# Kernel optimization log

Hardware: AMD Instinct MI355X
Metric: run time of the kernel (lower is better)

The kernel has to match this reference:

```python
import jax, jax.numpy as jnp
import numpy as np

B, C, T_TEXT, T_FEAT = 32, 256, 512, 2048
DELTA = 0.1  # self.temperature


def setup_inputs() -> dict:
    key = jax.random.key(0)
    k1, k2 = jax.random.split(key)
    x = jax.random.normal(k1, (B, C, T_TEXT), dtype=jnp.float32)
    # token durations in frames, ~U[0, 8): avg ~4 frames/token -> T_FEAT ~ 2048
    w = jax.random.uniform(k2, (B, T_TEXT), dtype=jnp.float32) * 8.0
    x_mask = jnp.ones((B, T_TEXT), dtype=bool)
    y_mask = jnp.ones((B, T_FEAT), dtype=bool)
    return {"x": x, "w": w, "x_mask": x_mask, "y_mask": y_mask}


def reference(x, w, x_mask, y_mask):
    # Gaussian upsampling (arXiv 2010.04301) with fixed temperature DELTA.
    # x: (B, C, T_text), w: (B, T_text), x_mask: (B, T_text), y_mask: (B, T_feat)
    T_feats = y_mask.shape[-1]
    # frame time indices, zeroed where y_mask is False
    t = jnp.arange(T_feats, dtype=jnp.float32)[None, :] * y_mask.astype(jnp.float32)  # (B, T_feat)
    # Gaussian centers: cumulative duration minus half of own duration
    c = jnp.cumsum(w, axis=-1) - 0.5 * w  # (B, T_text)
    # energy: -delta * (t - c)^2  -> (B, T_feat, T_text)
    energy = -DELTA * (t[:, :, None] - c[:, None, :]) ** 2
    # mask out padded text tokens
    energy = jnp.where(x_mask[:, None, :], energy, -jnp.inf)
    p_attn = jax.nn.softmax(energy, axis=-1)  # (B, T_feat, T_text)
    # weighted sum over text tokens: (B, C, T_feat)
    out = jnp.einsum("btn,bcn->bct", p_attn, x)
    return out
```

## Files before the change

kernel.cpp:

```cpp
#include <hip/hip_runtime.h>
#include <hip/hip_bf16.h>

#define B_    32
#define C_    256
#define NT    512
#define TFEAT 2048
#define TT    32
#define UW    96
#define PRE   32
#define DELTA 0.1f
#define PSTR  104
#define TPB   2
#define NGRP  32
#define TSTR  36

typedef __attribute__((ext_vector_type(4))) float f32x4;
typedef __attribute__((ext_vector_type(8))) unsigned short u16x8;
typedef __attribute__((ext_vector_type(8))) __bf16 bf16x8;

static __device__ inline unsigned short f2bfbits(float f) {
    __bf16 h = (__bf16)f;
    return __builtin_bit_cast(unsigned short, h);
}
static __device__ inline float bf2f(unsigned short h) {
    return __uint_as_float(((unsigned)h) << 16);
}

__global__ __launch_bounds__(256, 2) void fused_kernel(const float* __restrict__ x,
                                                       const float* __restrict__ w,
                                                       float* __restrict__ out) {
    __shared__ float cs[NT];
    __shared__ float wsum[8];
    __shared__ unsigned short Pt[TT][PSTR];
    __shared__ float Sinv[TT];
    __shared__ int sLO[TPB];
    __shared__ float trans[4][16][TSTR];

    int tid  = threadIdx.x;
    int bx   = blockIdx.x;
    int b    = bx & 31;
    int grp  = bx >> 5;
    int lane = tid & 63;
    int wv   = tid >> 6;

    float v0 = w[b * NT + tid];
    float v1 = w[b * NT + 256 + tid];
    float s0 = v0, s1 = v1;
#pragma unroll
    for (int off = 1; off < 64; off <<= 1) {
        float t0 = __shfl_up(s0, off);
        float t1 = __shfl_up(s1, off);
        if (lane >= off) { s0 += t0; s1 += t1; }
    }
    if (lane == 63) { wsum[wv] = s0; wsum[4 + wv] = s1; }
    __syncthreads();
    float pre0 = 0.f;
    float pre1 = wsum[0] + wsum[1] + wsum[2] + wsum[3];
#pragma unroll
    for (int i = 0; i < 4; ++i) if (i < wv) pre0 += wsum[i];
#pragma unroll
    for (int i = 0; i < 4; ++i) if (i < wv) pre1 += wsum[4 + i];
    cs[tid]       = pre0 + s0 - 0.5f * v0;
    cs[256 + tid] = pre1 + s1 - 0.5f * v1;
    __syncthreads();

    if (wv == 0) {
        int gid = lane >> 4;
        int k   = lane & 15;
        if (gid < TPB) {
            float ft = (float)((grp * TPB + gid) * TT);
            bool p = cs[32 * k + 31] < ft;
            unsigned long long m = __ballot(p);
            int K = __popcll((m >> (gid * 16)) & 0xFFFFull);
            int n;
            if (K >= 16) {
                n = NT;
            } else {
                int base = 32 * K;
                bool pa = cs[base + k] < ft;
                bool pb = cs[base + 16 + k] < ft;
                unsigned long long ma = __ballot(pa);
                unsigned long long mb = __ballot(pb);
                n = base + __popcll((ma >> (gid * 16)) & 0xFFFFull)
                         + __popcll((mb >> (gid * 16)) & 0xFFFFull);
            }
            if (k == 0) {
                int n1 = n < NT - 1 ? n : NT - 1;
                int n0 = n - 1 > 0 ? n - 1 : 0;
                int nstar = (fabsf(ft - cs[n0]) <= fabsf(ft - cs[n1])) ? n0 : n1;
                int L = (nstar - PRE) & ~3;
                if (L < 0) L = 0;
                if (L > NT - UW) L = NT - UW;
                sLO[gid] = L;
            }
        }
    }
    __syncthreads();

    int g = tid >> 3, j = tid & 7;
    int arow = lane & 15, kg = lane >> 4;
    int rr = lane >> 3, tq = lane & 7;

    for (int it = 0; it < TPB; ++it) {
        {
            int LO = sLO[it];
            float ft = (float)((grp * TPB + it) * TT + g);
            float e[12];
            float mx = -1e30f;
#pragma unroll
            for (int k = 0; k < 12; ++k) {
                float d = ft - cs[LO + j + 8 * k];
                e[k] = -DELTA * d * d;
                mx = fmaxf(mx, e[k]);
            }
            mx = fmaxf(mx, __shfl_xor(mx, 1));
            mx = fmaxf(mx, __shfl_xor(mx, 2));
            mx = fmaxf(mx, __shfl_xor(mx, 4));
            float sum = 0.f;
#pragma unroll
            for (int k = 0; k < 12; ++k) {
                unsigned short pbv = f2bfbits(__expf(e[k] - mx));
                sum += bf2f(pbv);
                Pt[g][j + 8 * k] = pbv;
            }
            sum += __shfl_xor(sum, 1);
            sum += __shfl_xor(sum, 2);
            sum += __shfl_xor(sum, 4);
            if (j == 0) Sinv[g] = 1.f / fmaxf(sum, 1e-30f);
        }
        __syncthreads();

        int LO = sLO[it];

        bf16x8 pfrag[2][3];
#pragma unroll
        for (int tt = 0; tt < 2; ++tt)
#pragma unroll
            for (int ks = 0; ks < 3; ++ks)
                pfrag[tt][ks] = __builtin_bit_cast(bf16x8,
                    *reinterpret_cast<const u16x8*>(
                        &Pt[tt * 16 + arow][ks * 32 + kg * 8]));

        f32x4 acc[2][4];
#pragma unroll
        for (int tt = 0; tt < 2; ++tt)
#pragma unroll
            for (int m = 0; m < 4; ++m)
                acc[tt][m] = (f32x4){0.f, 0.f, 0.f, 0.f};

        const float* xb = x + ((size_t)b * C_) * NT + LO + kg * 8;
#pragma unroll
        for (int m = 0; m < 4; ++m) {
            const float* xr = xb + (size_t)(wv * 64 + m * 16 + arow) * NT;
            bf16x8 xf[3];
#pragma unroll
            for (int ks = 0; ks < 3; ++ks) {
                f32x4 a0 = *reinterpret_cast<const f32x4*>(xr + ks * 32);
                f32x4 a1 = *reinterpret_cast<const f32x4*>(xr + ks * 32 + 4);
                bf16x8 vv;
#pragma unroll
                for (int q = 0; q < 4; ++q) {
                    vv[q]     = (__bf16)a0[q];
                    vv[q + 4] = (__bf16)a1[q];
                }
                xf[ks] = vv;
            }
#pragma unroll
            for (int tt = 0; tt < 2; ++tt)
#pragma unroll
                for (int ks = 0; ks < 3; ++ks)
                    acc[tt][m] = __builtin_amdgcn_mfma_f32_16x16x32_bf16(
                        pfrag[tt][ks], xf[ks], acc[tt][m], 0, 0, 0);
        }

        int t0f = (grp * TPB + it) * TT;
        float* ob = out + ((size_t)b * C_) * TFEAT + t0f;
        f32x4 sv0 = *reinterpret_cast<const f32x4*>(&Sinv[kg * 4]);
        f32x4 sv1 = *reinterpret_cast<const f32x4*>(&Sinv[16 + kg * 4]);
#pragma unroll
        for (int m = 0; m < 4; ++m) {
            *reinterpret_cast<f32x4*>(&trans[wv][arow][kg * 4])      = acc[0][m] * sv0;
            *reinterpret_cast<f32x4*>(&trans[wv][arow][16 + kg * 4]) = acc[1][m] * sv1;
            f32x4 o0 = *reinterpret_cast<const f32x4*>(&trans[wv][rr][tq * 4]);
            f32x4 o1 = *reinterpret_cast<const f32x4*>(&trans[wv][8 + rr][tq * 4]);
            int c0 = wv * 64 + m * 16;
            *reinterpret_cast<f32x4*>(ob + (size_t)(c0 + rr) * TFEAT + tq * 4)     = o0;
            *reinterpret_cast<f32x4*>(ob + (size_t)(c0 + 8 + rr) * TFEAT + tq * 4) = o1;
        }
        __syncthreads();
    }
}

extern "C" void kernel_launch(void* const* d_in, const int* in_sizes, int n_in,
                              void* d_out, int out_size, void* d_ws, size_t ws_size,
                              hipStream_t stream) {
    const float* x = (const float*)d_in[0];
    const float* w = (const float*)d_in[1];
    float* out = (float*)d_out;

    hipLaunchKernelGGL(fused_kernel, dim3(B_ * NGRP), dim3(256), 0, stream,
                       x, w, out);
}
```

Before: 34.86 us.

## Split into attention-weight kernel and GEMM kernel with x cached in LDS

Splits the fused kernel into two launches. The first computes the normalized banded bf16 attention weights and window offsets per 32-frame tile and writes them to workspace. The second keeps a 16-channel slab of x for a batch in shared memory as bf16 and loops over all 64 tiles. It reads the precomputed weights and writes output through an LDS staging buffer with nontemporal stores. This removes the old kernel's repeated per-tile global reads and bf16 conversion of x, at the cost of an extra launch and a workspace round trip for the weights. If the workspace is too small, it falls back to the old fused kernel.

```diff
diff --git a/kernel.cpp b/kernel.cpp
--- a/kernel.cpp
+++ b/kernel.cpp
@@ -10,25 +10,229 @@
 #define PRE   32
 #define DELTA 0.1f
 #define PSTR  104
+#define XSTR  520
+#define OSTR  516
+
+#define PHAT_ELEMS ((size_t)B_ * 64 * TT * UW)
+#define WS_NEED (PHAT_ELEMS * 2 + (size_t)B_ * 64 * 4)
+
+typedef __attribute__((ext_vector_type(4))) float f32x4;
+typedef __attribute__((ext_vector_type(8))) unsigned short u16x8;
+typedef __attribute__((ext_vector_type(8))) __bf16 bf16x8;
+
+static __device__ inline unsigned short f2bfbits(float f) {
+    __bf16 h = (__bf16)f;
+    return __builtin_bit_cast(unsigned short, h);
+}
+static __device__ inline float bf2f(unsigned short h) {
+    return __uint_as_float(((unsigned)h) << 16);
+}
+
+__global__ __launch_bounds__(256, 2) void p_kernel(const float* __restrict__ w,
+                                                   unsigned short* __restrict__ phat,
+                                                   int* __restrict__ lotab) {
+    __shared__ float cs[NT];
+    __shared__ float wsum[8];
+    __shared__ unsigned short Pt[TT][PSTR];
+    __shared__ int sLO[4];
+
+    int tid  = threadIdx.x;
+    int bx   = blockIdx.x;
+    int b    = bx & 31;
+    int tg   = bx >> 5;
+    int lane = tid & 63;
+    int wv   = tid >> 6;
+
+    float v0 = w[b * NT + tid];
+    float v1 = w[b * NT + 256 + tid];
+    float s0 = v0, s1 = v1;
+#pragma unroll
+    for (int off = 1; off < 64; off <<= 1) {
+        float t0 = __shfl_up(s0, off);
+        float t1 = __shfl_up(s1, off);
+        if (lane >= off) { s0 += t0; s1 += t1; }
+    }
+    if (lane == 63) { wsum[wv] = s0; wsum[4 + wv] = s1; }
+    __syncthreads();
+    float pre0 = 0.f;
+    float pre1 = wsum[0] + wsum[1] + wsum[2] + wsum[3];
+#pragma unroll
+    for (int i = 0; i < 4; ++i) if (i < wv) pre0 += wsum[i];
+#pragma unroll
+    for (int i = 0; i < 4; ++i) if (i < wv) pre1 += wsum[4 + i];
+    cs[tid]       = pre0 + s0 - 0.5f * v0;
+    cs[256 + tid] = pre1 + s1 - 0.5f * v1;
+    __syncthreads();
+
+    if (wv == 0) {
+        int gid = lane >> 4;
+        int k   = lane & 15;
+        float ft = (float)((tg * 4 + gid) * TT);
+        bool p = cs[32 * k + 31] < ft;
+        unsigned long long m = __ballot(p);
+        int K = __popcll((m >> (gid * 16)) & 0xFFFFull);
+        int n;
+        if (K >= 16) {
+            n = NT;
+        } else {
+            int base = 32 * K;
+            bool pa = cs[base + k] < ft;
+            bool pb = cs[base + 16 + k] < ft;
+            unsigned long long ma = __ballot(pa);
+            unsigned long long mb = __ballot(pb);
+            n = base + __popcll((ma >> (gid * 16)) & 0xFFFFull)
+                     + __popcll((mb >> (gid * 16)) & 0xFFFFull);
+        }
+        if (k == 0) {
+            int n1 = n < NT - 1 ? n : NT - 1;
+            int n0 = n - 1 > 0 ? n - 1 : 0;
+            int nstar = (fabsf(ft - cs[n0]) <= fabsf(ft - cs[n1])) ? n0 : n1;
+            int L = (nstar - PRE) & ~3;
+            if (L < 0) L = 0;
+            if (L > NT - UW) L = NT - UW;
+            sLO[gid] = L;
+            lotab[b * 64 + tg * 4 + gid] = L;
+        }
+    }
+    __syncthreads();
+
+    int g = tid >> 3, j = tid & 7;
+
+    for (int it = 0; it < 4; ++it) {
+        int tile = tg * 4 + it;
+        int LO = sLO[it];
+        float ft = (float)(tile * TT + g);
+        float e[12];
+        float mx = -1e30f;
+#pragma unroll
+        for (int k = 0; k < 12; ++k) {
+            float d = ft - cs[LO + j + 8 * k];
+            e[k] = -DELTA * d * d;
+            mx = fmaxf(mx, e[k]);
+        }
+        mx = fmaxf(mx, __shfl_xor(mx, 1));
+        mx = fmaxf(mx, __shfl_xor(mx, 2));
+        mx = fmaxf(mx, __shfl_xor(mx, 4));
+        float p[12];
+        float sum = 0.f;
+#pragma unroll
+        for (int k = 0; k < 12; ++k) {
+            p[k] = __expf(e[k] - mx);
+            sum += p[k];
+        }
+        sum += __shfl_xor(sum, 1);
+        sum += __shfl_xor(sum, 2);
+        sum += __shfl_xor(sum, 4);
+        float inv = 1.f / fmaxf(sum, 1e-30f);
+#pragma unroll
+        for (int k = 0; k < 12; ++k)
+            Pt[g][j + 8 * k] = f2bfbits(p[k] * inv);
+        __syncthreads();
+
+        const unsigned* pw = (const unsigned*)&Pt[0][0];
+        unsigned* gd = (unsigned*)phat + (size_t)(b * 64 + tile) * 1536 + tid * 6;
+        int a = tid >> 3, r6 = tid & 7;
+#pragma unroll
+        for (int q = 0; q < 6; ++q)
+            gd[q] = pw[a * (PSTR / 2) + r6 * 6 + q];
+        __syncthreads();
+    }
+}
+
+__global__ __launch_bounds__(256, 2) void g_kernel(const float* __restrict__ x,
+                                                   const unsigned short* __restrict__ phat,
+                                                   const int* __restrict__ lotab,
+                                                   float* __restrict__ out) {
+    __shared__ unsigned short xs[16][XSTR];
+    __shared__ float outbuf[16][OSTR];
+
+    int tid  = threadIdx.x;
+    int bx   = blockIdx.x;
+    int b    = bx & 31;
+    int cg   = bx >> 5;
+    int c0   = cg * 16;
+    int lane = tid & 63;
+    int w    = tid >> 6;
+
+    {
+        int c = tid >> 4, k = tid & 15;
+        const float* xr = x + ((size_t)(b * C_ + c0 + c)) * NT + k * 32;
+#pragma unroll
+        for (int jj = 0; jj < 4; ++jj) {
+            f32x4 a0 = *reinterpret_cast<const f32x4*>(xr + jj * 8);
+            f32x4 a1 = *reinterpret_cast<const f32x4*>(xr + jj * 8 + 4);
+            bf16x8 vv;
+#pragma unroll
+            for (int q = 0; q < 4; ++q) {
+                vv[q]     = (__bf16)a0[q];
+                vv[q + 4] = (__bf16)a1[q];
+            }
+            *reinterpret_cast<bf16x8*>(&xs[c][k * 32 + jj * 8]) = vv;
+        }
+    }
+    __syncthreads();
+
+    int cc = lane & 15;
+    int kg = lane >> 4;
+
+    for (int s = 0; s < 16; ++s) {
+        int tile = s * 4 + w;
+        int LO = lotab[b * 64 + tile];
+
+        const unsigned short* ap = phat + (size_t)(b * 64 + tile) * (TT * UW);
+        bf16x8 af[2][3];
+#pragma unroll
+        for (int mt = 0; mt < 2; ++mt)
+#pragma unroll
+            for (int ks = 0; ks < 3; ++ks)
+                af[mt][ks] = __builtin_bit_cast(bf16x8,
+                    *reinterpret_cast<const u16x8*>(
+                        ap + (mt * 16 + cc) * UW + ks * 32 + kg * 8));
+
+        bf16x8 bfg[3];
+#pragma unroll
+        for (int ks = 0; ks < 3; ++ks)
+            bfg[ks] = __builtin_bit_cast(bf16x8,
+                *reinterpret_cast<const u16x8*>(&xs[cc][LO + ks * 32 + kg * 8]));
+
+        f32x4 acc[2];
+        acc[0] = (f32x4){0.f, 0.f, 0.f, 0.f};
+        acc[1] = (f32x4){0.f, 0.f, 0.f, 0.f};
+#pragma unroll
+        for (int mt = 0; mt < 2; ++mt)
+#pragma unroll
+            for (int ks = 0; ks < 3; ++ks)
+                acc[mt] = __builtin_amdgcn_mfma_f32_16x16x32_bf16(
+                    af[mt][ks], bfg[ks], acc[mt], 0, 0, 0);
+
+        int toff = (s & 3) * 128 + w * 32 + kg * 4;
+#pragma unroll
+        for (int mt = 0; mt < 2; ++mt)
+            *reinterpret_cast<f32x4*>(&outbuf[cc][toff + mt * 16]) = acc[mt];
+
+        if ((s & 3) == 3) {
+            __syncthreads();
+            int row = tid >> 4, kk = tid & 15;
+            int tb = (s >> 2) * 512;
+            float* ob = out + ((size_t)(b * C_ + c0 + row)) * TFEAT + tb;
+#pragma unroll
+            for (int jj = 0; jj < 8; ++jj) {
+                f32x4 v = *reinterpret_cast<const f32x4*>(&outbuf[row][(kk + 16 * jj) * 4]);
+                __builtin_nontemporal_store(v,
+                    reinterpret_cast<f32x4*>(ob + (kk + 16 * jj) * 4));
+            }
+            __syncthreads();
+        }
+    }
+}
+
 #define TPB   2
 #define NGRP  32
 #define TSTR  36
 
-typedef __attribute__((ext_vector_type(4))) float f32x4;
-typedef __attribute__((ext_vector_type(8))) unsigned short u16x8;
-typedef __attribute__((ext_vector_type(8))) __bf16 bf16x8;
-
-static __device__ inline unsigned short f2bfbits(float f) {
-    __bf16 h = (__bf16)f;
-    return __builtin_bit_cast(unsigned short, h);
-}
-static __device__ inline float bf2f(unsigned short h) {
-    return __uint_as_float(((unsigned)h) << 16);
-}
-
-__global__ __launch_bounds__(256, 2) void fused_kernel(const float* __restrict__ x,
-                                                       const float* __restrict__ w,
-                                                       float* __restrict__ out) {
+__global__ __launch_bounds__(256, 2) void fused_fallback(const float* __restrict__ x,
+                                                         const float* __restrict__ w,
+                                                         float* __restrict__ out) {
     __shared__ float cs[NT];
     __shared__ float wsum[8];
     __shared__ unsigned short Pt[TT][PSTR];
@@ -131,7 +335,6 @@
         __syncthreads();
 
         int LO = sLO[it];
-
         bf16x8 pfrag[2][3];
 #pragma unroll
         for (int tt = 0; tt < 2; ++tt)
@@ -183,9 +386,9 @@
             *reinterpret_cast<f32x4*>(&trans[wv][arow][16 + kg * 4]) = acc[1][m] * sv1;
             f32x4 o0 = *reinterpret_cast<const f32x4*>(&trans[wv][rr][tq * 4]);
             f32x4 o1 = *reinterpret_cast<const f32x4*>(&trans[wv][8 + rr][tq * 4]);
-            int c0 = wv * 64 + m * 16;
-            *reinterpret_cast<f32x4*>(ob + (size_t)(c0 + rr) * TFEAT + tq * 4)     = o0;
-            *reinterpret_cast<f32x4*>(ob + (size_t)(c0 + 8 + rr) * TFEAT + tq * 4) = o1;
+            int cq = wv * 64 + m * 16;
+            *reinterpret_cast<f32x4*>(ob + (size_t)(cq + rr) * TFEAT + tq * 4)     = o0;
+            *reinterpret_cast<f32x4*>(ob + (size_t)(cq + 8 + rr) * TFEAT + tq * 4) = o1;
         }
         __syncthreads();
     }
@@ -198,6 +401,14 @@
     const float* w = (const float*)d_in[1];
     float* out = (float*)d_out;
 
-    hipLaunchKernelGGL(fused_kernel, dim3(B_ * NGRP), dim3(256), 0, stream,
-                       x, w, out);
-}
+    if (ws_size >= WS_NEED) {
+        unsigned short* phat = (unsigned short*)d_ws;
+        int* lotab = (int*)((char*)d_ws + PHAT_ELEMS * 2);
+        hipLaunchKernelGGL(p_kernel, dim3(B_ * 16), dim3(256), 0, stream, w, phat, lotab);
+        hipLaunchKernelGGL(g_kernel, dim3(B_ * 16), dim3(256), 0, stream,
+                           x, phat, lotab, out);
+    } else {
+        hipLaunchKernelGGL(fused_fallback, dim3(B_ * NGRP), dim3(256), 0, stream,
+                           x, w, out);
+    }
+}
```

New measurement: 39.14 us. 1.12x slower.
